# Optimization experiments

Hardware: AMD Instinct MI355X
Metric: run time of the kernel (lower is better)

Reference implementation:

```python
import jax, jax.numpy as jnp
import numpy as np

N_NODES = 50000
N_EDGES = 1600000
IN_C = 64
OUT_C = 64
N_CLASSES = 45


def setup_inputs() -> dict:
    key = jax.random.key(0)
    ks = jax.random.split(key, 12)

    def lin(k, i, o):
        return jax.random.normal(k, (i, o), jnp.float32) / np.float32(np.sqrt(i))

    return dict(
        x=jax.random.normal(ks[0], (N_NODES, IN_C), jnp.float32),
        edge_index=jax.random.randint(ks[1], (2, N_EDGES), 0, N_NODES, dtype=jnp.int32),
        W_z=lin(ks[2], IN_C, OUT_C), b_z=jnp.zeros((OUT_C,), jnp.float32),
        Wl_z=lin(ks[3], 2 * OUT_C, OUT_C), bl_z=jnp.zeros((OUT_C,), jnp.float32),
        W_r=lin(ks[4], IN_C, OUT_C), b_r=jnp.zeros((OUT_C,), jnp.float32),
        Wl_r=lin(ks[5], 2 * OUT_C, OUT_C), bl_r=jnp.zeros((OUT_C,), jnp.float32),
        W_h=lin(ks[6], IN_C, OUT_C), b_h=jnp.zeros((OUT_C,), jnp.float32),
        Wl_h=lin(ks[7], 2 * OUT_C, OUT_C), bl_h=jnp.zeros((OUT_C,), jnp.float32),
        W_out=lin(ks[8], OUT_C, N_CLASSES), b_out=jnp.zeros((N_CLASSES,), jnp.float32),
    )


def _gcn(x, W, b, src, dst, dinv):
    # GCNConv with improved self-loops (fill value 2.0):
    # out = D^{-1/2} (A + 2I) D^{-1/2} X W + b, with deg = in_degree + 2
    xw = x @ W                                   # [N, OUT_C]
    norm = dinv[src] * dinv[dst]                 # [E]
    agg = jax.ops.segment_sum(norm[:, None] * xw[src], dst, num_segments=N_NODES)
    agg = agg + (2.0 * dinv * dinv)[:, None] * xw  # self-loop contribution
    return agg + b


def reference(x, edge_index, W_z, b_z, Wl_z, bl_z, W_r, b_r, Wl_r, bl_r,
              W_h, b_h, Wl_h, bl_h, W_out, b_out):
    src, dst = edge_index[0], edge_index[1]
    deg = jax.ops.segment_sum(jnp.ones((N_EDGES,), jnp.float32), dst,
                              num_segments=N_NODES) + 2.0
    dinv = jax.lax.rsqrt(deg)

    # TGCN cell with H0 = 0 (no prior hidden state passed)
    H = jnp.zeros((N_NODES, OUT_C), x.dtype)
    Z = jax.nn.sigmoid(
        jnp.concatenate([_gcn(x, W_z, b_z, src, dst, dinv), H], axis=1) @ Wl_z + bl_z)
    R = jax.nn.sigmoid(
        jnp.concatenate([_gcn(x, W_r, b_r, src, dst, dinv), H], axis=1) @ Wl_r + bl_r)
    H_tilde = jnp.tanh(
        jnp.concatenate([_gcn(x, W_h, b_h, src, dst, dinv), H * R], axis=1) @ Wl_h + bl_h)
    H = Z * H + (1.0 - Z) * H_tilde

    # relu + linear readout to 45 classes
    return jax.nn.relu(H) @ W_out + b_out
```

## Files before the change

### kernel.cpp

```cpp
#include <hip/hip_runtime.h>

#define N_NODES 50000
#define N_EDGES 1600000
#define NB 782
#define NBB 256
#define CHUNK 6250
#define CAP 2560
#define SCAP 3072
#define ZROW 50000
#define NTILES 3125

typedef unsigned short ushort_t;
typedef _Float16 v8h __attribute__((ext_vector_type(8)));
typedef _Float16 v4h __attribute__((ext_vector_type(4)));
typedef _Float16 v2h __attribute__((ext_vector_type(2)));
typedef float f32x4_t __attribute__((ext_vector_type(4)));


__global__ __launch_bounds__(256) void k_binw(
    const int* __restrict__ ei, int* __restrict__ gcur, int* __restrict__ bins,
    const float* __restrict__ Wz, const float* __restrict__ bz,
    const float* __restrict__ Wlz, const float* __restrict__ blz,
    const float* __restrict__ Wh, const float* __restrict__ bh,
    const float* __restrict__ Wlh, const float* __restrict__ blh,
    const float* __restrict__ Wout, float* __restrict__ B2f,
    _Float16* __restrict__ Bzh, _Float16* __restrict__ Bwo) {
  __shared__ int arena[8320];
  int tid = threadIdx.x, blk = blockIdx.x;
  if (blk < NBB) {
    int* h    = arena;
    int* segb = arena + NB;
    int* pk   = arena + 2 * NB;
    for (int i = tid; i < NB; i += 256) h[i] = 0;
    __syncthreads();
    const int2* s2 = (const int2*)(ei + blk * CHUNK);
    const int2* d2 = (const int2*)(ei + N_EDGES + blk * CHUNK);
    for (int i = tid; i < CHUNK / 2; i += 256) {
      int2 s = s2[i];
      int2 d = d2[i];
      pk[2 * i]     = s.x | ((d.x & 63) << 16) | ((d.x >> 6) << 22);
      pk[2 * i + 1] = s.y | ((d.y & 63) << 16) | ((d.y >> 6) << 22);
      atomicAdd(&h[d.x >> 6], 1);
      atomicAdd(&h[d.y >> 6], 1);
    }
    __syncthreads();
    for (int b = tid; b < NB; b += 256) {
      int c = h[b];
      segb[b] = c ? atomicAdd(&gcur[b], c) : 0;
      h[b] = 0;
    }
    __syncthreads();
    for (int i = tid; i < CHUNK; i += 256) {
      int v = pk[i];
      int b = (unsigned)v >> 22;
      int p = atomicAdd(&h[b], 1);
      bins[b * CAP + segb[b] + p] = v & 0x3FFFFF;
    }
  } else {
    int wblk = blk - NBB;
    float* A  = (float*)arena;
    float* Bm = (float*)(arena + 4160);
    bool zpath = wblk < 4;
    const float* Wsrc = zpath ? Wz : Wh;
    const float* Lsrc = zpath ? Wlz : Wlh;
    for (int idx = tid; idx < 4096; idx += 256) {
      A[(idx >> 6) * 65 + (idx & 63)] = Wsrc[idx];
      Bm[(idx >> 6) * 65 + (idx & 63)] = Lsrc[idx];
    }
    __syncthreads();
    int lane = (tid >> 1) & 63;
    int j0 = (tid & 1) * 4;
    int ks = (tid >> 7) & 1;
    int k0 = ks * 32 + ((lane >> 4) << 3) + j0;
    int col = (wblk & 3) * 16 + (lane & 15);
    float a0 = 0.f, a1 = 0.f, a2 = 0.f, a3 = 0.f;
    for (int q = 0; q < 64; ++q) {
      float bv = Bm[q * 65 + col];
      a0 = fmaf(A[k0 * 65 + q], bv, a0);
      a1 = fmaf(A[(k0 + 1) * 65 + q], bv, a1);
      a2 = fmaf(A[(k0 + 2) * 65 + q], bv, a2);
      a3 = fmaf(A[(k0 + 3) * 65 + q], bv, a3);
    }
    int tb = wblk * 1024 + tid * 4;
    v4h o; o[0] = (_Float16)a0; o[1] = (_Float16)a1;
    o[2] = (_Float16)a2; o[3] = (_Float16)a3;
    *(v4h*)(Bzh + tb) = o;
    if ((wblk == 0 || wblk == 4) && tid < 64) {
      float v = zpath ? blz[tid] : blh[tid];
      const float* bb = zpath ? bz : bh;
      for (int q = 0; q < 64; ++q) v = fmaf(bb[q], Bm[q * 65 + tid], v);
      B2f[tid * 2 + (zpath ? 0 : 1)] = v;
    }
    if (wblk == 1) {
      for (int e2 = 0; e2 < 12; ++e2) {
        int t2 = tid * 12 + e2;
        int ln = (t2 >> 3) & 63, j = t2 & 7;
        int ntile = t2 >> 10, ks2 = (t2 >> 9) & 1;
        int n = ntile * 16 + (ln & 15);
        int k = ks2 * 32 + ((ln >> 4) << 3) + j;
        Bwo[t2] = (_Float16)((n < 45) ? Wout[k * 45 + n] : 0.f);
      }
    }
  }
}

__global__ __launch_bounds__(256, 4) void k_sort(
    const int* __restrict__ bins, const int* __restrict__ gcur,
    const float* __restrict__ x,
    ushort_t* __restrict__ srcp, int2* __restrict__ rowiv,
    float* __restrict__ dinv, _Float16* __restrict__ xp) {
  __shared__ int dg[64], lo[64], cur[64];
  __shared__ float sdin[64];
  __shared__ int Tsh;
  __shared__ ushort_t buf[8192];
  int tid = threadIdx.x, b = blockIdx.x;
  int start = b * CAP, end = start + gcur[b];
  if (tid < 64) dg[tid] = 0;
  __syncthreads();
  for (int i = start + tid; i < end; i += 256)
    atomicAdd(&dg[bins[i] >> 16], 1);
  __syncthreads();
  int pdv = 0;
  if (tid < 64) { pdv = (dg[tid] + 7) & ~7; lo[tid] = pdv; }
  __syncthreads();
  for (int off = 1; off < 64; off <<= 1) {
    int u = 0;
    if (tid < 64 && tid >= off) u = lo[tid - off];
    __syncthreads();
    if (tid < 64) lo[tid] += u;
    __syncthreads();
  }
  int ex = 0;
  if (tid < 64) {
    ex = lo[tid] - pdv;
    cur[tid] = ex;
    if (tid == 63) Tsh = lo[63];
  }
  __syncthreads();
  int T = Tsh;
  int base = b * SCAP;
  for (int i = tid; i < T; i += 256) buf[i] = (ushort_t)ZROW;
  __syncthreads();
  for (int i = start + tid; i < end; i += 256) {
    int v = bins[i];
    int dl = v >> 16;
    int p = atomicAdd(&cur[dl], 1);
    buf[p] = (ushort_t)(v & 0xFFFF);
  }
  __syncthreads();
  for (int i = tid; i < T; i += 256) srcp[base + i] = buf[i];
  if (tid < 64) {
    int v = b * 64 + tid;
    if (v < N_NODES) {
      rowiv[v] = make_int2(base + ex, pdv);
      float dv = rsqrtf((float)dg[tid] + 2.0f);
      dinv[v] = dv;
      sdin[tid] = dv;
    } else {
      sdin[tid] = 0.f;
    }
  }
  __syncthreads();
  const float4* x4 = (const float4*)x;
  int base4 = b * 1024;
  int nb64 = b * 4096;
  for (int idx = tid; idx < 1024; idx += 256) {
    int row = idx >> 4;
    int v = b * 64 + row;
    if (v < N_NODES) {
      float4 xv = x4[base4 + idx];
      float s = sdin[row];
      v4h o;
      o[0] = (_Float16)(s * xv.x); o[1] = (_Float16)(s * xv.y);
      o[2] = (_Float16)(s * xv.z); o[3] = (_Float16)(s * xv.w);
      *(v4h*)(xp + nb64 + idx * 4) = o;
    }
  }
  if (b == 0 && tid < 64) xp[ZROW * 64 + tid] = (_Float16)0.f;
}

__global__ __launch_bounds__(256, 8) void k_agg(
    const ushort_t* __restrict__ srcp, const int2* __restrict__ rowiv,
    const float* __restrict__ dinv, const _Float16* __restrict__ xp,
    _Float16* __restrict__ sxg) {
  int tid = threadIdx.x;
  int lane = tid & 63;
  int grp = lane >> 3;
  int chOff = (lane & 7) << 3;
  const v2h onE = {(_Float16)1.0f, (_Float16)0.0f};
  const v2h onO = {(_Float16)0.0f, (_Float16)1.0f};
  int w = blockIdx.x * 4 + (tid >> 6);
  int nw = gridDim.x * 4;
  for (int v = w; v < N_NODES; v += nw) {
    int vu = __builtin_amdgcn_readfirstlane(v);
    int2 ri = rowiv[vu];
    int beg = ri.x, pd = ri.y;
    float aE[2][4], aO[2][4];
    #pragma unroll
    for (int j = 0; j < 4; ++j) {
      aE[0][j] = 0.f; aE[1][j] = 0.f; aO[0][j] = 0.f; aO[1][j] = 0.f;
    }
    int e = beg, eend = beg + pd;
    for (; e + 32 <= eend; e += 32) {
      int s0 = (int)srcp[e + grp];
      int s1 = (int)srcp[e + 8 + grp];
      int s2 = (int)srcp[e + 16 + grp];
      int s3 = (int)srcp[e + 24 + grp];
      v8h r0 = *(const v8h*)(xp + (s0 << 6) + chOff);
      v8h r1 = *(const v8h*)(xp + (s1 << 6) + chOff);
      v8h r2 = *(const v8h*)(xp + (s2 << 6) + chOff);
      v8h r3 = *(const v8h*)(xp + (s3 << 6) + chOff);
      const v2h* p0 = (const v2h*)&r0;
      const v2h* p1 = (const v2h*)&r1;
      const v2h* p2 = (const v2h*)&r2;
      const v2h* p3 = (const v2h*)&r3;
      #pragma unroll
      for (int j = 0; j < 4; ++j) {
        aE[0][j] = __builtin_amdgcn_fdot2(p0[j], onE, aE[0][j], false);
        aO[0][j] = __builtin_amdgcn_fdot2(p0[j], onO, aO[0][j], false);
        aE[1][j] = __builtin_amdgcn_fdot2(p1[j], onE, aE[1][j], false);
        aO[1][j] = __builtin_amdgcn_fdot2(p1[j], onO, aO[1][j], false);
        aE[0][j] = __builtin_amdgcn_fdot2(p2[j], onE, aE[0][j], false);
        aO[0][j] = __builtin_amdgcn_fdot2(p2[j], onO, aO[0][j], false);
        aE[1][j] = __builtin_amdgcn_fdot2(p3[j], onE, aE[1][j], false);
        aO[1][j] = __builtin_amdgcn_fdot2(p3[j], onO, aO[1][j], false);
      }
    }
    for (; e < eend; e += 8) {
      int s0 = (int)srcp[e + grp];
      v8h r0 = *(const v8h*)(xp + (s0 << 6) + chOff);
      const v2h* p0 = (const v2h*)&r0;
      #pragma unroll
      for (int j = 0; j < 4; ++j) {
        aE[0][j] = __builtin_amdgcn_fdot2(p0[j], onE, aE[0][j], false);
        aO[0][j] = __builtin_amdgcn_fdot2(p0[j], onO, aO[0][j], false);
      }
    }
    float a[8];
    #pragma unroll
    for (int j = 0; j < 4; ++j) {
      a[2 * j]     = aE[0][j] + aE[1][j];
      a[2 * j + 1] = aO[0][j] + aO[1][j];
    }
    #pragma unroll
    for (int j = 0; j < 8; ++j) {
      a[j] += __shfl_xor(a[j], 8);
      a[j] += __shfl_xor(a[j], 16);
      a[j] += __shfl_xor(a[j], 32);
    }
    if (lane < 8) {
      float dv = dinv[vu];
      v8h self = *(const v8h*)(xp + (vu << 6) + chOff);
      v8h o;
      #pragma unroll
      for (int j = 0; j < 8; ++j)
        o[j] = (_Float16)(dv * a[j] + 2.f * dv * (float)self[j]);
      *(v8h*)(sxg + (vu << 6) + chOff) = o;
    }
  }
}

__global__ __launch_bounds__(256) void k_cell(
    const _Float16* __restrict__ sxg, const _Float16* __restrict__ Bzh,
    const _Float16* __restrict__ Bwo, const float2* __restrict__ B2,
    const float* __restrict__ bout, float* __restrict__ out) {
  __shared__ __align__(16) _Float16 tbuf[4][16][72];
  int tid = threadIdx.x;
  int lane = tid & 63, wv = tid >> 6;
  int l15 = lane & 15, quad = lane >> 4;
  int tile = blockIdx.x * 4 + wv;
  if (tile >= NTILES) return;

  v8h bzf[8][2], bwf[3][2];
  #pragma unroll
  for (int t = 0; t < 8; ++t)
    #pragma unroll
    for (int ks = 0; ks < 2; ++ks)
      bzf[t][ks] = *(const v8h*)(Bzh + (((t * 2 + ks) * 64 + lane) << 3));
  #pragma unroll
  for (int t = 0; t < 3; ++t)
    #pragma unroll
    for (int ks = 0; ks < 2; ++ks)
      bwf[t][ks] = *(const v8h*)(Bwo + (((t * 2 + ks) * 64 + lane) << 3));
  float zb[4], hb[4], ob[3];
  #pragma unroll
  for (int t = 0; t < 4; ++t) {
    float2 bb = B2[t * 16 + l15];
    zb[t] = bb.x; hb[t] = bb.y;
  }
  #pragma unroll
  for (int t = 0; t < 3; ++t) {
    int c = t * 16 + l15;
    ob[t] = (c < 45) ? bout[c] : 0.f;
  }

  const _Float16* ar = sxg + (tile * 16 + l15) * 64 + quad * 8;
  v8h a0 = *(const v8h*)ar;
  v8h a1 = *(const v8h*)(ar + 32);

  f32x4_t accz[8];
  #pragma unroll
  for (int t = 0; t < 8; ++t) {
    f32x4_t c4 = {0.f, 0.f, 0.f, 0.f};
    c4 = __builtin_amdgcn_mfma_f32_16x16x32_f16(a0, bzf[t][0], c4, 0, 0, 0);
    c4 = __builtin_amdgcn_mfma_f32_16x16x32_f16(a1, bzf[t][1], c4, 0, 0, 0);
    accz[t] = c4;
  }

  #pragma unroll
  for (int t = 0; t < 4; ++t) {
    #pragma unroll
    for (int r = 0; r < 4; ++r) {
      float zv = accz[t][r] + zb[t];
      float hv = accz[t + 4][r] + hb[t];
      float Z = 1.f / (1.f + __expf(-zv));
      float tt = fminf(15.f, fmaxf(-15.f, hv));
      float e2 = __expf(-2.f * tt);
      float Th = (1.f - e2) / (1.f + e2);
      tbuf[wv][quad * 4 + r][t * 16 + l15] = (_Float16)fmaxf((1.f - Z) * Th, 0.f);
    }
  }
  __asm__ volatile("s_waitcnt lgkmcnt(0)" ::: "memory");

  v8h p0 = *(const v8h*)&tbuf[wv][l15][quad * 8];
  v8h p1 = *(const v8h*)&tbuf[wv][l15][32 + quad * 8];

  #pragma unroll
  for (int t = 0; t < 3; ++t) {
    f32x4_t o4 = {0.f, 0.f, 0.f, 0.f};
    o4 = __builtin_amdgcn_mfma_f32_16x16x32_f16(p0, bwf[t][0], o4, 0, 0, 0);
    o4 = __builtin_amdgcn_mfma_f32_16x16x32_f16(p1, bwf[t][1], o4, 0, 0, 0);
    int c = t * 16 + l15;
    if (c < 45) {
      #pragma unroll
      for (int r = 0; r < 4; ++r)
        out[(tile * 16 + quad * 4 + r) * 45 + c] = o4[r] + ob[t];
    }
  }
}

extern "C" void kernel_launch(void* const* d_in, const int* in_sizes, int n_in,
                              void* d_out, int out_size, void* d_ws, size_t ws_size,
                              hipStream_t stream) {
  const float* x    = (const float*)d_in[0];
  const int*   ei   = (const int*)d_in[1];
  const float* Wz   = (const float*)d_in[2];
  const float* bz   = (const float*)d_in[3];
  const float* Wlz  = (const float*)d_in[4];
  const float* blz  = (const float*)d_in[5];
  const float* Wh   = (const float*)d_in[10];
  const float* bh   = (const float*)d_in[11];
  const float* Wlh  = (const float*)d_in[12];
  const float* blh  = (const float*)d_in[13];
  const float* Wout = (const float*)d_in[14];
  const float* bout = (const float*)d_in[15];
  float* out = (float*)d_out;

  char* w = (char*)d_ws;
  int*      bins  = (int*)(w + 0);
  _Float16* sxg   = (_Float16*)(w + 0);
  int*      gcur  = (int*)(w + 8007680);
  ushort_t* srcp  = (ushort_t*)(w + 8010816);
  int2*     rowiv = (int2*)(w + 12815424);
  float*    dinv  = (float*)(w + 13215424);
  float2*   B2    = (float2*)(w + 13415424);
  _Float16* Bzh   = (_Float16*)(w + 13415936);
  _Float16* Bwo   = (_Float16*)(w + 13432320);
  _Float16* xp    = (_Float16*)(w + 13438464);

  hipMemsetAsync(gcur, 0, NB * sizeof(int), stream);
  k_binw <<<NBB + 8, 256, 0, stream>>>(ei, gcur, bins, Wz, bz, Wlz, blz,
                                       Wh, bh, Wlh, blh, Wout,
                                       (float*)B2, Bzh, Bwo);
  k_sort <<<NB, 256, 0, stream>>>(bins, gcur, x, srcp, rowiv, dinv, xp);
  k_agg  <<<2048, 256, 0, stream>>>(srcp, rowiv, dinv, xp, sxg);
  k_cell <<<NB, 256, 0, stream>>>(sxg, Bzh, Bwo, B2, bout, out);
}
```

Before: 157.1 us.

## Process two nodes per wavefront in aggregation with padded zero-row edges

The aggregation kernel now splits each 64-lane wavefront into two halves, each gathering one destination node, and loads both row descriptors with a single int4 read. The loop runs to the larger degree of the pair, and out-of-range edges are redirected to a zero row, so the separate tail loop is gone. This aims to cut per-node overhead and divergence for average degree around 32, at the cost of wasted gathers when paired nodes differ in degree.

```diff
diff --git a/kernel.cpp b/kernel.cpp
--- a/kernel.cpp
+++ b/kernel.cpp
@@ -185,27 +185,35 @@
     _Float16* __restrict__ sxg) {
   int tid = threadIdx.x;
   int lane = tid & 63;
-  int grp = lane >> 3;
+  int half = lane >> 5;
+  int grp = (lane & 31) >> 3;
   int chOff = (lane & 7) << 3;
   const v2h onE = {(_Float16)1.0f, (_Float16)0.0f};
   const v2h onO = {(_Float16)0.0f, (_Float16)1.0f};
   int w = blockIdx.x * 4 + (tid >> 6);
   int nw = gridDim.x * 4;
-  for (int v = w; v < N_NODES; v += nw) {
-    int vu = __builtin_amdgcn_readfirstlane(v);
-    int2 ri = rowiv[vu];
-    int beg = ri.x, pd = ri.y;
+  const int4* rv4 = (const int4*)rowiv;
+  for (int vb = w * 2; vb < N_NODES; vb += nw * 2) {
+    int vu = vb + half;
+    int4 rp = rv4[vb >> 1];
+    int beg = half ? rp.z : rp.x;
+    int pd  = half ? rp.w : rp.y;
+    int pdm = max(pd, __shfl_xor(pd, 32));
+    const ushort_t* sp = srcp + beg;
     float aE[2][4], aO[2][4];
     #pragma unroll
     for (int j = 0; j < 4; ++j) {
       aE[0][j] = 0.f; aE[1][j] = 0.f; aO[0][j] = 0.f; aO[1][j] = 0.f;
     }
-    int e = beg, eend = beg + pd;
-    for (; e + 32 <= eend; e += 32) {
-      int s0 = (int)srcp[e + grp];
-      int s1 = (int)srcp[e + 8 + grp];
-      int s2 = (int)srcp[e + 16 + grp];
-      int s3 = (int)srcp[e + 24 + grp];
+    for (int off = 0; off < pdm; off += 16) {
+      int e0 = off + grp;
+      int e1 = off + 4 + grp;
+      int e2 = off + 8 + grp;
+      int e3 = off + 12 + grp;
+      int s0 = (e0 < pd) ? (int)sp[e0] : ZROW;
+      int s1 = (e1 < pd) ? (int)sp[e1] : ZROW;
+      int s2 = (e2 < pd) ? (int)sp[e2] : ZROW;
+      int s3 = (e3 < pd) ? (int)sp[e3] : ZROW;
       v8h r0 = *(const v8h*)(xp + (s0 << 6) + chOff);
       v8h r1 = *(const v8h*)(xp + (s1 << 6) + chOff);
       v8h r2 = *(const v8h*)(xp + (s2 << 6) + chOff);
@@ -226,16 +234,6 @@
         aO[1][j] = __builtin_amdgcn_fdot2(p3[j], onO, aO[1][j], false);
       }
     }
-    for (; e < eend; e += 8) {
-      int s0 = (int)srcp[e + grp];
-      v8h r0 = *(const v8h*)(xp + (s0 << 6) + chOff);
-      const v2h* p0 = (const v2h*)&r0;
-      #pragma unroll
-      for (int j = 0; j < 4; ++j) {
-        aE[0][j] = __builtin_amdgcn_fdot2(p0[j], onE, aE[0][j], false);
-        aO[0][j] = __builtin_amdgcn_fdot2(p0[j], onO, aO[0][j], false);
-      }
-    }
     float a[8];
     #pragma unroll
     for (int j = 0; j < 4; ++j) {
@@ -246,9 +244,8 @@
     for (int j = 0; j < 8; ++j) {
       a[j] += __shfl_xor(a[j], 8);
       a[j] += __shfl_xor(a[j], 16);
-      a[j] += __shfl_xor(a[j], 32);
-    }
-    if (lane < 8) {
+    }
+    if ((lane & 31) < 8) {
       float dv = dinv[vu];
       v8h self = *(const v8h*)(xp + (vu << 6) + chOff);
       v8h o;
```

New measurement: 161.6 us. 2.9% more time.
